# Kernel tuning notes

Measured on AMD Instinct MI355X. Metric: run time of the kernel, lower is better.

Reference implementation:

```python
import jax, jax.numpy as jnp
import numpy as np


def setup_inputs() -> dict:
    key = jax.random.key(0)
    x = jax.random.normal(key, (32, 256, 128, 128), dtype=jnp.float32)
    return {"x": x}


def reference(x):
    b, c, h, w = x.shape
    # global average pool over spatial dims, per (b, c)
    pooled = jnp.mean(x, axis=(2, 3), keepdims=True)          # [b, c, 1, 1]
    # xn = (x * pooled).mean over channels -> [b, 1, h, w]
    xn = jnp.mean(x * pooled, axis=1, keepdims=True)
    # mean over batch -> [h, w]
    entro = jnp.mean(xn, axis=0)[0]
    e = entro.reshape(-1)
    emin = jnp.min(e)
    emax = jnp.max(e)
    e = (e - emin) / (emax - emin) * 255.0
    # torch.histc(bins=256, min=0, max=255): 256 uniform bins, last bin
    # right-inclusive -> matches jnp.histogram semantics.
    his, _ = jnp.histogram(e, bins=256, range=(0.0, 255.0))
    his = jax.lax.stop_gradient(his.astype(x.dtype)) / (h * w)
    entro_final = jnp.sum(his * -jnp.log(his + 1e-8))
    nz = jnp.count_nonzero(his).astype(x.dtype)
    entro_final = entro_final / nz
    s = jnp.mean(jax.nn.sigmoid(xn))
    return s + entro_final * 10.0
```

## Files before the change

### kernel.cpp

```cpp
#include <hip/hip_runtime.h>
#include <math.h>

#define BB 32
#define CC 256
#define HW 16384
#define HW4 4096
#define BC (BB*CC)

#define XN_OFF    8192
#define ENTRO_OFF (XN_OFF + 4*BB*HW)
#define SIG_OFF   (ENTRO_OFF + HW)

__global__ __launch_bounds__(256) void pool_kernel(const float* __restrict__ x,
                                                   float* __restrict__ ws) {
    const int bc = blockIdx.x;
    const int t  = threadIdx.x;
    const float4* xv = (const float4*)x + (size_t)bc * HW4;
    float s = 0.f;
#pragma unroll
    for (int i = 0; i < 16; ++i) {
        float4 v = xv[t + i * 256];
        s += v.x + v.y + v.z + v.w;
    }
    for (int o = 32; o > 0; o >>= 1) s += __shfl_down(s, o);
    __shared__ float part[4];
    if ((t & 63) == 0) part[t >> 6] = s;
    __syncthreads();
    if (t == 0) {
        float tot = part[0] + part[1] + part[2] + part[3];
        ws[bc] = tot * (1.0f / HW);
    }
    if (bc == 0 && t == 0) ws[SIG_OFF] = 0.f;
}

__global__ __launch_bounds__(256) void xn_partial_kernel(const float* __restrict__ x,
                                                         float* __restrict__ ws) {
    const int bid   = blockIdx.x;
    const int cg    = bid & 3;
    const int chunk = (bid >> 2) & 15;
    const int b     = bid >> 6;
    const int t     = threadIdx.x;

    __shared__ float spool[64];
    if (t < 64) spool[t] = ws[b * CC + cg * 64 + t];
    __syncthreads();

    const float4* xv = (const float4*)x;
    const size_t base = (size_t)b * CC * HW4 + (size_t)(cg * 64) * HW4
                      + (size_t)chunk * 256 + t;

    float ax = 0.f, ay = 0.f, az = 0.f, aw = 0.f;
#pragma unroll 8
    for (int c = 0; c < 64; ++c) {
        float4 v = xv[base + (size_t)c * HW4];
        float p = spool[c];
        ax += v.x * p; ay += v.y * p; az += v.z * p; aw += v.w * p;
    }
    float4 o; o.x = ax; o.y = ay; o.z = az; o.w = aw;
    float4* xnp = (float4*)(ws + XN_OFF);
    xnp[(size_t)(cg * BB + b) * HW4 + chunk * 256 + t] = o;
}

__global__ __launch_bounds__(256) void entro_sig_kernel(float* __restrict__ ws) {
    const int j = blockIdx.x * 256 + threadIdx.x;
    const int t = threadIdx.x;
    const float4* xnp = (const float4*)(ws + XN_OFF);
    const float inv_c = 1.0f / CC;

    float ex = 0.f, ey = 0.f, ez = 0.f, ew = 0.f;
    float sg = 0.f;
#pragma unroll 4
    for (int b = 0; b < BB; ++b) {
        float4 s0 = xnp[(size_t)(0 * BB + b) * HW4 + j];
        float4 s1 = xnp[(size_t)(1 * BB + b) * HW4 + j];
        float4 s2 = xnp[(size_t)(2 * BB + b) * HW4 + j];
        float4 s3 = xnp[(size_t)(3 * BB + b) * HW4 + j];
        float xnx = (s0.x + s1.x + s2.x + s3.x) * inv_c;
        float xny = (s0.y + s1.y + s2.y + s3.y) * inv_c;
        float xnz = (s0.z + s1.z + s2.z + s3.z) * inv_c;
        float xnw = (s0.w + s1.w + s2.w + s3.w) * inv_c;
        ex += xnx; ey += xny; ez += xnz; ew += xnw;
        sg += 1.f / (1.f + expf(-xnx)) + 1.f / (1.f + expf(-xny)) +
              1.f / (1.f + expf(-xnz)) + 1.f / (1.f + expf(-xnw));
    }
    const float inv_b = 1.0f / BB;
    float4 e; e.x = ex * inv_b; e.y = ey * inv_b; e.z = ez * inv_b; e.w = ew * inv_b;
    ((float4*)(ws + ENTRO_OFF))[j] = e;

    for (int o = 32; o > 0; o >>= 1) sg += __shfl_down(sg, o);
    __shared__ float part[4];
    if ((t & 63) == 0) part[t >> 6] = sg;
    __syncthreads();
    if (t == 0) {
        float tot = part[0] + part[1] + part[2] + part[3];
        atomicAdd(&ws[SIG_OFF], tot);
    }
}

__global__ __launch_bounds__(256) void finalize_kernel(const float* __restrict__ ws,
                                                       float* __restrict__ out) {
    const int t = threadIdx.x;
    const float4* ev = (const float4*)(ws + ENTRO_OFF);

    float lmin = INFINITY, lmax = -INFINITY;
#pragma unroll
    for (int i = 0; i < 16; ++i) {
        float4 v = ev[t + i * 256];
        lmin = fminf(lmin, fminf(fminf(v.x, v.y), fminf(v.z, v.w)));
        lmax = fmaxf(lmax, fmaxf(fmaxf(v.x, v.y), fmaxf(v.z, v.w)));
    }
    for (int o = 32; o > 0; o >>= 1) {
        lmin = fminf(lmin, __shfl_down(lmin, o));
        lmax = fmaxf(lmax, __shfl_down(lmax, o));
    }
    __shared__ float smin[4], smax[4];
    __shared__ float bmin, bmax;
    if ((t & 63) == 0) { smin[t >> 6] = lmin; smax[t >> 6] = lmax; }
    __syncthreads();
    if (t == 0) {
        bmin = fminf(fminf(smin[0], smin[1]), fminf(smin[2], smin[3]));
        bmax = fmaxf(fmaxf(smax[0], smax[1]), fmaxf(smax[2], smax[3]));
    }
    __shared__ unsigned int hist[256];
    hist[t] = 0u;
    __syncthreads();

    const float emin = bmin, emax = bmax;
    const float scale = 256.0f / (emax - emin);
#pragma unroll
    for (int i = 0; i < 16; ++i) {
        float4 v = ev[t + i * 256];
        int i0 = (int)floorf((v.x - emin) * scale);
        int i1 = (int)floorf((v.y - emin) * scale);
        int i2 = (int)floorf((v.z - emin) * scale);
        int i3 = (int)floorf((v.w - emin) * scale);
        i0 = i0 < 0 ? 0 : (i0 > 255 ? 255 : i0);
        i1 = i1 < 0 ? 0 : (i1 > 255 ? 255 : i1);
        i2 = i2 < 0 ? 0 : (i2 > 255 ? 255 : i2);
        i3 = i3 < 0 ? 0 : (i3 > 255 ? 255 : i3);
        atomicAdd(&hist[i0], 1u);
        atomicAdd(&hist[i1], 1u);
        atomicAdd(&hist[i2], 1u);
        atomicAdd(&hist[i3], 1u);
    }
    __syncthreads();

    const unsigned int h = hist[t];
    const float his = (float)h * (1.0f / HW);
    float term = (h > 0u) ? his * (-logf(his + 1e-8f)) : 0.f;
    float nzf  = (h > 0u) ? 1.f : 0.f;
    for (int o = 32; o > 0; o >>= 1) {
        term += __shfl_down(term, o);
        nzf  += __shfl_down(nzf, o);
    }
    __shared__ float sterm[4], snz[4];
    if ((t & 63) == 0) { sterm[t >> 6] = term; snz[t >> 6] = nzf; }
    __syncthreads();
    if (t == 0) {
        float ent = sterm[0] + sterm[1] + sterm[2] + sterm[3];
        float nz  = snz[0] + snz[1] + snz[2] + snz[3];
        float sig = ws[SIG_OFF] * (1.0f / ((float)BB * (float)HW));
        out[0] = sig + (ent / nz) * 10.0f;
    }
}

extern "C" void kernel_launch(void* const* d_in, const int* in_sizes, int n_in,
                              void* d_out, int out_size, void* d_ws, size_t ws_size,
                              hipStream_t stream) {
    const float* x = (const float*)d_in[0];
    float* out = (float*)d_out;
    float* ws  = (float*)d_ws;

    pool_kernel<<<BC, 256, 0, stream>>>(x, ws);
    xn_partial_kernel<<<BB * 16 * 4, 256, 0, stream>>>(x, ws);
    entro_sig_kernel<<<16, 256, 0, stream>>>(ws);
    finalize_kernel<<<1, 256, 0, stream>>>(ws, out);
}
```

Baseline: 793.0 us.

## Fuse channel pooling and weighted channel sum into a single pass over input

Replaces the separate pooling and weighted-sum kernels with one kernel. Each block owns 16 channels of one batch, computes each channel's spatial mean with a block reduction, and accumulates mean-weighted values in registers, so the input is read once instead of twice. Partials over 16 channel groups are written out and reduced by a combine kernel that now splits the batch across four thread quarters. This adds more partial-buffer traffic, a combine step with only 16 blocks, and per-channel block barriers.

```diff
diff --git a/kernel.cpp b/kernel.cpp
--- a/kernel.cpp
+++ b/kernel.cpp
@@ -5,94 +5,111 @@
 #define CC 256
 #define HW 16384
 #define HW4 4096
-#define BC (BB*CC)
+#define CG 16
+#define CPG 16
 
-#define XN_OFF    8192
-#define ENTRO_OFF (XN_OFF + 4*BB*HW)
+#define XNP_OFF   0
+#define ENTRO_OFF (CG*BB*HW)
 #define SIG_OFF   (ENTRO_OFF + HW)
 
-__global__ __launch_bounds__(256) void pool_kernel(const float* __restrict__ x,
-                                                   float* __restrict__ ws) {
-    const int bc = blockIdx.x;
-    const int t  = threadIdx.x;
-    const float4* xv = (const float4*)x + (size_t)bc * HW4;
-    float s = 0.f;
-#pragma unroll
-    for (int i = 0; i < 16; ++i) {
-        float4 v = xv[t + i * 256];
-        s += v.x + v.y + v.z + v.w;
+__global__ __launch_bounds__(1024) void fused_kernel(const float* __restrict__ x,
+                                                     float* __restrict__ ws) {
+    const int bid = blockIdx.x;
+    const int b   = bid >> 4;
+    const int cg  = bid & 15;
+    const int t   = threadIdx.x;
+    const int wid = t >> 6;
+    const int lane = t & 63;
+
+    if (bid == 0 && t == 0) ws[SIG_OFF] = 0.f;
+
+    const float4* xv = (const float4*)x + ((size_t)b * CC + (size_t)cg * CPG) * HW4;
+
+    __shared__ float wsum[16];
+    __shared__ float smean;
+
+    float4 a0 = {0,0,0,0}, a1 = {0,0,0,0}, a2 = {0,0,0,0}, a3 = {0,0,0,0};
+
+    for (int c = 0; c < CPG; ++c) {
+        const float4* p = xv + (size_t)c * HW4;
+        float4 v0 = p[t];
+        float4 v1 = p[t + 1024];
+        float4 v2 = p[t + 2048];
+        float4 v3 = p[t + 3072];
+
+        float s = v0.x + v0.y + v0.z + v0.w
+                + v1.x + v1.y + v1.z + v1.w
+                + v2.x + v2.y + v2.z + v2.w
+                + v3.x + v3.y + v3.z + v3.w;
+        for (int o = 32; o > 0; o >>= 1) s += __shfl_down(s, o);
+        if (lane == 0) wsum[wid] = s;
+        __syncthreads();
+        if (t < 16) {
+            float ss = wsum[t];
+            for (int o = 8; o > 0; o >>= 1) ss += __shfl_down(ss, o);
+            if (t == 0) smean = ss * (1.0f / HW);
+        }
+        __syncthreads();
+        const float m = smean;
+        a0.x += m * v0.x; a0.y += m * v0.y; a0.z += m * v0.z; a0.w += m * v0.w;
+        a1.x += m * v1.x; a1.y += m * v1.y; a1.z += m * v1.z; a1.w += m * v1.w;
+        a2.x += m * v2.x; a2.y += m * v2.y; a2.z += m * v2.z; a2.w += m * v2.w;
+        a3.x += m * v3.x; a3.y += m * v3.y; a3.z += m * v3.z; a3.w += m * v3.w;
     }
-    for (int o = 32; o > 0; o >>= 1) s += __shfl_down(s, o);
-    __shared__ float part[4];
-    if ((t & 63) == 0) part[t >> 6] = s;
-    __syncthreads();
-    if (t == 0) {
-        float tot = part[0] + part[1] + part[2] + part[3];
-        ws[bc] = tot * (1.0f / HW);
-    }
-    if (bc == 0 && t == 0) ws[SIG_OFF] = 0.f;
+
+    float4* xnp = (float4*)(ws + XNP_OFF) + ((size_t)cg * BB + b) * HW4;
+    xnp[t]        = a0;
+    xnp[t + 1024] = a1;
+    xnp[t + 2048] = a2;
+    xnp[t + 3072] = a3;
 }
 
-__global__ __launch_bounds__(256) void xn_partial_kernel(const float* __restrict__ x,
-                                                         float* __restrict__ ws) {
-    const int bid   = blockIdx.x;
-    const int cg    = bid & 3;
-    const int chunk = (bid >> 2) & 15;
-    const int b     = bid >> 6;
-    const int t     = threadIdx.x;
-
-    __shared__ float spool[64];
-    if (t < 64) spool[t] = ws[b * CC + cg * 64 + t];
-    __syncthreads();
-
-    const float4* xv = (const float4*)x;
-    const size_t base = (size_t)b * CC * HW4 + (size_t)(cg * 64) * HW4
-                      + (size_t)chunk * 256 + t;
-
-    float ax = 0.f, ay = 0.f, az = 0.f, aw = 0.f;
-#pragma unroll 8
-    for (int c = 0; c < 64; ++c) {
-        float4 v = xv[base + (size_t)c * HW4];
-        float p = spool[c];
-        ax += v.x * p; ay += v.y * p; az += v.z * p; aw += v.w * p;
-    }
-    float4 o; o.x = ax; o.y = ay; o.z = az; o.w = aw;
-    float4* xnp = (float4*)(ws + XN_OFF);
-    xnp[(size_t)(cg * BB + b) * HW4 + chunk * 256 + t] = o;
-}
-
-__global__ __launch_bounds__(256) void entro_sig_kernel(float* __restrict__ ws) {
-    const int j = blockIdx.x * 256 + threadIdx.x;
-    const int t = threadIdx.x;
-    const float4* xnp = (const float4*)(ws + XN_OFF);
+__global__ __launch_bounds__(1024) void combine_kernel(float* __restrict__ ws) {
+    const int t  = threadIdx.x;
+    const int jl = t & 255;
+    const int j  = blockIdx.x * 256 + jl;
+    const int bq = t >> 8;
+    const float4* xnp = (const float4*)(ws + XNP_OFF);
     const float inv_c = 1.0f / CC;
 
-    float ex = 0.f, ey = 0.f, ez = 0.f, ew = 0.f;
-    float sg = 0.f;
-#pragma unroll 4
-    for (int b = 0; b < BB; ++b) {
-        float4 s0 = xnp[(size_t)(0 * BB + b) * HW4 + j];
-        float4 s1 = xnp[(size_t)(1 * BB + b) * HW4 + j];
-        float4 s2 = xnp[(size_t)(2 * BB + b) * HW4 + j];
-        float4 s3 = xnp[(size_t)(3 * BB + b) * HW4 + j];
-        float xnx = (s0.x + s1.x + s2.x + s3.x) * inv_c;
-        float xny = (s0.y + s1.y + s2.y + s3.y) * inv_c;
-        float xnz = (s0.z + s1.z + s2.z + s3.z) * inv_c;
-        float xnw = (s0.w + s1.w + s2.w + s3.w) * inv_c;
+    float ex = 0.f, ey = 0.f, ez = 0.f, ew = 0.f, sg = 0.f;
+    for (int bb = 0; bb < 8; ++bb) {
+        const int b = bq * 8 + bb;
+        float ax = 0.f, ay = 0.f, az = 0.f, aw = 0.f;
+#pragma unroll
+        for (int cg = 0; cg < CG; ++cg) {
+            float4 s = xnp[((size_t)cg * BB + b) * HW4 + j];
+            ax += s.x; ay += s.y; az += s.z; aw += s.w;
+        }
+        float xnx = ax * inv_c, xny = ay * inv_c, xnz = az * inv_c, xnw = aw * inv_c;
         ex += xnx; ey += xny; ez += xnz; ew += xnw;
         sg += 1.f / (1.f + expf(-xnx)) + 1.f / (1.f + expf(-xny)) +
               1.f / (1.f + expf(-xnz)) + 1.f / (1.f + expf(-xnw));
     }
-    const float inv_b = 1.0f / BB;
-    float4 e; e.x = ex * inv_b; e.y = ey * inv_b; e.z = ez * inv_b; e.w = ew * inv_b;
-    ((float4*)(ws + ENTRO_OFF))[j] = e;
+
+    __shared__ float4 epart[4][256];
+    float4 ep; ep.x = ex; ep.y = ey; ep.z = ez; ep.w = ew;
+    epart[bq][jl] = ep;
+    __syncthreads();
+    if (bq == 0) {
+        float4 e0 = epart[0][jl], e1 = epart[1][jl], e2 = epart[2][jl], e3 = epart[3][jl];
+        const float inv_b = 1.0f / BB;
+        float4 e;
+        e.x = (e0.x + e1.x + e2.x + e3.x) * inv_b;
+        e.y = (e0.y + e1.y + e2.y + e3.y) * inv_b;
+        e.z = (e0.z + e1.z + e2.z + e3.z) * inv_b;
+        e.w = (e0.w + e1.w + e2.w + e3.w) * inv_b;
+        ((float4*)(ws + ENTRO_OFF))[j] = e;
+    }
 
     for (int o = 32; o > 0; o >>= 1) sg += __shfl_down(sg, o);
-    __shared__ float part[4];
+    __shared__ float part[16];
     if ((t & 63) == 0) part[t >> 6] = sg;
     __syncthreads();
     if (t == 0) {
-        float tot = part[0] + part[1] + part[2] + part[3];
+        float tot = 0.f;
+#pragma unroll
+        for (int i = 0; i < 16; ++i) tot += part[i];
         atomicAdd(&ws[SIG_OFF], tot);
     }
 }
@@ -171,8 +188,7 @@
     float* out = (float*)d_out;
     float* ws  = (float*)d_ws;
 
-    pool_kernel<<<BC, 256, 0, stream>>>(x, ws);
-    xn_partial_kernel<<<BB * 16 * 4, 256, 0, stream>>>(x, ws);
-    entro_sig_kernel<<<16, 256, 0, stream>>>(ws);
+    fused_kernel<<<BB * CG, 1024, 0, stream>>>(x, ws);
+    combine_kernel<<<16, 1024, 0, stream>>>(ws);
     finalize_kernel<<<1, 256, 0, stream>>>(ws, out);
 }
```

Result: faster. 701.4 us (-11.5%).
